# Kernel optimization log

Hardware: AMD Instinct MI355X
Metric: run time of the kernel (lower is better)

Reference implementation:

```python
import jax, jax.numpy as jnp
import numpy as np

B, S, D, H = 4, 2048, 1024, 16
DH = D // H  # 64
EPS = 1e-6


def _phi(t):
    # positive feature map used by linear attention: elu(x) + 1
    return jax.nn.elu(t) + 1.0


def setup_inputs() -> dict:
    key = jax.random.key(0)
    ks = jax.random.split(key, 5)
    scale = 1.0 / np.sqrt(D)
    return {
        "x": jax.random.normal(ks[0], (B, S, D), dtype=jnp.float32),
        "Wq": jax.random.normal(ks[1], (D, D), dtype=jnp.float32) * scale,
        "Wk": jax.random.normal(ks[2], (D, D), dtype=jnp.float32) * scale,
        "Wv": jax.random.normal(ks[3], (D, D), dtype=jnp.float32) * scale,
        "Wo": jax.random.normal(ks[4], (D, D), dtype=jnp.float32) * scale,
    }


def reference(x, Wq, Wk, Wv, Wo):
    b, s, d = x.shape
    # projections -> [b, s, H, DH]
    q = _phi((x @ Wq).reshape(b, s, H, DH))
    k = _phi((x @ Wk).reshape(b, s, H, DH))
    v = (x @ Wv).reshape(b, s, H, DH)

    # time-major for scan: [s, b, H, DH]
    qT = jnp.moveaxis(q, 1, 0)
    kT = jnp.moveaxis(k, 1, 0)
    vT = jnp.moveaxis(v, 1, 0)

    S0 = jnp.zeros((b, H, DH, DH), dtype=x.dtype)  # matrix memory per head
    z0 = jnp.zeros((b, H, DH), dtype=x.dtype)      # normalizer per head

    def step(carry, qkv):
        Smat, z = carry
        qt, kt, vt = qkv
        Smat = Smat + kt[..., :, None] * vt[..., None, :]  # [b,H,DH,DH]
        z = z + kt
        num = jnp.einsum('bhd,bhde->bhe', qt, Smat)
        den = jnp.einsum('bhd,bhd->bh', qt, z)
        out = num / (den[..., None] + EPS)
        return (Smat, z), out

    _, outs = jax.lax.scan(step, (S0, z0), (qT, kT, vT))  # [s,b,H,DH]
    out = jnp.moveaxis(outs, 0, 1).reshape(b, s, d)
    return out @ Wo
```

## Files before the change

kernel.cpp:

```cpp
#include <hip/hip_runtime.h>
#include <hip/hip_bf16.h>
#include <math.h>

constexpr int Bb  = 4;
constexpr int SEQ = 2048;
constexpr int Dd  = 1024;
constexpr int Hh  = 16;
constexpr int DHh = 64;
constexpr int Cc  = 64;
constexpr int NCc = SEQ / Cc;
constexpr int Mm  = Bb * SEQ;
constexpr float EPSf = 1e-6f;

typedef __attribute__((ext_vector_type(8))) short bf16x8;
typedef __attribute__((ext_vector_type(4))) float f32x4;
typedef __attribute__((ext_vector_type(8))) unsigned short u16x8;

__device__ __forceinline__ float bf2f(unsigned short u) {
    return __uint_as_float((unsigned)u << 16);
}
__device__ __forceinline__ unsigned short f2bf(float f) {
    unsigned u = __float_as_uint(f);
    unsigned r = u + 0x7fff + ((u >> 16) & 1);
    return (unsigned short)(r >> 16);
}
__device__ __forceinline__ int swz(int row, int col) {
    return col ^ (((row >> 3) & 7) << 3);
}

__global__ __launch_bounds__(256)
void cast_bf16(const float* __restrict__ in, unsigned short* __restrict__ out, int n8) {
    int i = blockIdx.x * 256 + threadIdx.x;
    if (i >= n8) return;
    const float4* p = reinterpret_cast<const float4*>(in) + (size_t)i * 2;
    float4 a = p[0], b = p[1];
    u16x8 o;
    o[0] = f2bf(a.x); o[1] = f2bf(a.y); o[2] = f2bf(a.z); o[3] = f2bf(a.w);
    o[4] = f2bf(b.x); o[5] = f2bf(b.y); o[6] = f2bf(b.z); o[7] = f2bf(b.w);
    *(reinterpret_cast<u16x8*>(out) + i) = o;
}

__global__ __launch_bounds__(256)
void transpose_cast_w(const float* __restrict__ W0, const float* __restrict__ W1,
                      const float* __restrict__ W2, const float* __restrict__ W3,
                      unsigned short* __restrict__ WT) {
    const float* W = (blockIdx.z == 0) ? W0 : (blockIdx.z == 1) ? W1
                     : (blockIdx.z == 2) ? W2 : W3;
    unsigned short* T = WT + (size_t)blockIdx.z * Dd * Dd;
    __shared__ float t[64][65];
    const int r0 = blockIdx.y * 64, c0 = blockIdx.x * 64;
    const int tid = threadIdx.x;
    const int lr = tid >> 4, lc4 = (tid & 15) * 4;
#pragma unroll
    for (int it = 0; it < 4; ++it) {
        int row = lr + it * 16;
        float4 v = *reinterpret_cast<const float4*>(W + (size_t)(r0 + row) * Dd + c0 + lc4);
        t[row][lc4 + 0] = v.x; t[row][lc4 + 1] = v.y;
        t[row][lc4 + 2] = v.z; t[row][lc4 + 3] = v.w;
    }
    __syncthreads();
#pragma unroll
    for (int it = 0; it < 4; ++it) {
        int col = lr + it * 16;
        ushort4 o;
        o.x = f2bf(t[lc4 + 0][col]); o.y = f2bf(t[lc4 + 1][col]);
        o.z = f2bf(t[lc4 + 2][col]); o.w = f2bf(t[lc4 + 3][col]);
        *reinterpret_cast<ushort4*>(T + (size_t)(c0 + col) * Dd + r0 + lc4) = o;
    }
}

template<int QKV>
__global__ __launch_bounds__(512, 1)
void gemm_pipe(const unsigned short* __restrict__ A, const unsigned short* __restrict__ BT,
               float* __restrict__ outF, unsigned short* __restrict__ oQ,
               unsigned short* __restrict__ oK, unsigned short* __restrict__ oV) {
    constexpr int Kd  = 1024;
    constexpr int BK  = 64;
    constexpr int NT  = Kd / BK;
    constexpr int GX  = QKV ? 12 : 4;
    constexpr int NWG = GX * 64;
    constexpr int BUFSZ = (128 + 256) * BK;

    __shared__ __align__(16) unsigned short lds[3 * BUFSZ];

    const int wg0 = blockIdx.x;
    const int wg  = (wg0 & 7) * (NWG >> 3) + (wg0 >> 3);
    const int by = wg & 63, bx = wg >> 6;
    const int row0 = by * 128;
    const int col0 = bx * 256;

    const int tid  = threadIdx.x;
    const int lane = tid & 63;
    const int wave = tid >> 6;
    const int wm = (wave >> 2) * 64;
    const int wn = (wave & 3) * 64;
    const int fr = lane & 15;
    const int hi = lane >> 4;

    f32x4 acc[4][4];
#pragma unroll
    for (int mf = 0; mf < 4; ++mf)
#pragma unroll
        for (int nf = 0; nf < 4; ++nf) acc[mf][nf] = (f32x4){0.f, 0.f, 0.f, 0.f};

    auto stage1 = [&](int sel, int kt, int l) {
        unsigned short* base = &lds[sel * BUFSZ];
        int seg = l * 512 + tid;
        if (l < 2) {
            int row = seg >> 3, sp = seg & 7;
            int gcol = kt + ((sp ^ (row & 7)) << 3);
            __builtin_amdgcn_global_load_lds(
                (const __attribute__((address_space(1))) void*)(A + (size_t)(row0 + row) * Kd + gcol),
                (__attribute__((address_space(3))) void*)(base + seg * 8), 16, 0, 0);
        } else {
            int bseg = seg - 1024;
            int row = bseg >> 3, sp = bseg & 7;
            int gcol = kt + ((sp ^ (row & 7)) << 3);
            __builtin_amdgcn_global_load_lds(
                (const __attribute__((address_space(1))) void*)(BT + (size_t)(col0 + row) * Kd + gcol),
                (__attribute__((address_space(3))) void*)(base + 8192 + bseg * 8), 16, 0, 0);
        }
    };
    auto lda = [&](const unsigned short* bufA, int mf, int ks) {
        int row = wm + mf * 16 + fr;
        int sp = ((ks << 2) | hi) ^ (row & 7);
        return *reinterpret_cast<const bf16x8*>(bufA + row * 64 + sp * 8);
    };
    auto ldb = [&](const unsigned short* bufB, int nf, int ks) {
        int row = wn + nf * 16 + fr;
        int sp = ((ks << 2) | hi) ^ (row & 7);
        return *reinterpret_cast<const bf16x8*>(bufB + row * 64 + sp * 8);
    };

#pragma unroll
    for (int l = 0; l < 6; ++l) stage1(0, 0, l);
#pragma unroll
    for (int l = 0; l < 6; ++l) stage1(1, BK, l);

    int selc = 0;
    for (int t = 0; t < NT; ++t) {
        if (t < NT - 1) { asm volatile("s_waitcnt vmcnt(6)" ::: "memory"); }
        else            { asm volatile("s_waitcnt vmcnt(0)" ::: "memory"); }
        __builtin_amdgcn_sched_barrier(0);
        __builtin_amdgcn_s_barrier();
        __builtin_amdgcn_sched_barrier(0);

        const unsigned short* bufA = &lds[selc * BUFSZ];
        const unsigned short* bufB = bufA + 8192;
        int sels = selc + 2; if (sels >= 3) sels -= 3;
        const bool st = (t + 2 < NT);
        const int kt2 = (t + 2) * BK;

        bf16x8 a0_[4], a1_[4], bL[2], bM[2], bN[2], bO[2];

#pragma unroll
        for (int mf = 0; mf < 4; ++mf) a0_[mf] = lda(bufA, mf, 0);
        bL[0] = ldb(bufB, 0, 0); bL[1] = ldb(bufB, 1, 0);
        bM[0] = ldb(bufB, 2, 0); bM[1] = ldb(bufB, 3, 0);

        asm volatile("s_waitcnt lgkmcnt(2)" ::: "memory");
        __builtin_amdgcn_sched_barrier(0);
        __builtin_amdgcn_s_setprio(1);
#pragma unroll
        for (int mf = 0; mf < 4; ++mf) {
            acc[mf][0] = __builtin_amdgcn_mfma_f32_16x16x32_bf16(a0_[mf], bL[0], acc[mf][0], 0, 0, 0);
            acc[mf][1] = __builtin_amdgcn_mfma_f32_16x16x32_bf16(a0_[mf], bL[1], acc[mf][1], 0, 0, 0);
        }
        __builtin_amdgcn_s_setprio(0);

#pragma unroll
        for (int mf = 0; mf < 4; ++mf) a1_[mf] = lda(bufA, mf, 1);
        bN[0] = ldb(bufB, 0, 1); bN[1] = ldb(bufB, 1, 1);
        if (st) { stage1(sels, kt2, 0); stage1(sels, kt2, 1); stage1(sels, kt2, 2); }

        asm volatile("s_waitcnt lgkmcnt(6)" ::: "memory");
        __builtin_amdgcn_sched_barrier(0);
        __builtin_amdgcn_s_setprio(1);
#pragma unroll
        for (int mf = 0; mf < 4; ++mf) {
            acc[mf][2] = __builtin_amdgcn_mfma_f32_16x16x32_bf16(a0_[mf], bM[0], acc[mf][2], 0, 0, 0);
            acc[mf][3] = __builtin_amdgcn_mfma_f32_16x16x32_bf16(a0_[mf], bM[1], acc[mf][3], 0, 0, 0);
        }
        __builtin_amdgcn_s_setprio(0);

        bO[0] = ldb(bufB, 2, 1); bO[1] = ldb(bufB, 3, 1);
        if (st) { stage1(sels, kt2, 3); stage1(sels, kt2, 4); stage1(sels, kt2, 5); }

        asm volatile("s_waitcnt lgkmcnt(2)" ::: "memory");
        __builtin_amdgcn_sched_barrier(0);
        __builtin_amdgcn_s_setprio(1);
#pragma unroll
        for (int mf = 0; mf < 4; ++mf) {
            acc[mf][0] = __builtin_amdgcn_mfma_f32_16x16x32_bf16(a1_[mf], bN[0], acc[mf][0], 0, 0, 0);
            acc[mf][1] = __builtin_amdgcn_mfma_f32_16x16x32_bf16(a1_[mf], bN[1], acc[mf][1], 0, 0, 0);
        }
        __builtin_amdgcn_s_setprio(0);

        asm volatile("s_waitcnt lgkmcnt(0)" ::: "memory");
        __builtin_amdgcn_sched_barrier(0);
        __builtin_amdgcn_s_setprio(1);
#pragma unroll
        for (int mf = 0; mf < 4; ++mf) {
            acc[mf][2] = __builtin_amdgcn_mfma_f32_16x16x32_bf16(a1_[mf], bO[0], acc[mf][2], 0, 0, 0);
            acc[mf][3] = __builtin_amdgcn_mfma_f32_16x16x32_bf16(a1_[mf], bO[1], acc[mf][3], 0, 0, 0);
        }
        __builtin_amdgcn_s_setprio(0);

        selc = (selc == 2) ? 0 : selc + 1;
    }

    if (QKV) {
        const int sel = col0 >> 10;
        unsigned short* ob = (sel == 0) ? oQ : (sel == 1) ? oK : oV;
        const bool phi = (sel < 2);
        const int ncol0 = col0 & 1023;
#pragma unroll
        for (int mf = 0; mf < 4; ++mf)
#pragma unroll
            for (int nf = 0; nf < 4; ++nf)
#pragma unroll
                for (int r = 0; r < 4; ++r) {
                    int orow = row0 + wm + mf * 16 + hi * 4 + r;
                    int ocol = ncol0 + wn + nf * 16 + fr;
                    float v = acc[mf][nf][r];
                    if (phi) v = (v > 0.f) ? (v + 1.f) : __expf(v);
                    ob[(size_t)orow * Dd + ocol] = f2bf(v);
                }
    } else {
#pragma unroll
        for (int mf = 0; mf < 4; ++mf)
#pragma unroll
            for (int nf = 0; nf < 4; ++nf)
#pragma unroll
                for (int r = 0; r < 4; ++r) {
                    int orow = row0 + wm + mf * 16 + hi * 4 + r;
                    int ocol = col0 + wn + nf * 16 + fr;
                    outF[(size_t)orow * Dd + ocol] = acc[mf][nf][r];
                }
    }
}

__global__ __launch_bounds__(256)
void chunk_sums_mfma(const unsigned short* __restrict__ Kb, const unsigned short* __restrict__ Vb,
                     unsigned short* __restrict__ CSb, float* __restrict__ CZ) {
    const int blk = blockIdx.x;
    const int c  = blk & (NCc - 1);
    const int bh = blk >> 5;
    const int b  = bh >> 4;
    const int h  = bh & 15;
    const int tid  = threadIdx.x;
    const int wave = tid >> 6, lane = tid & 63;
    const int lo = lane & 15, hi = lane >> 4;
    const int wr = (wave >> 1) * 32, wc = (wave & 1) * 32;

    __shared__ __align__(16) unsigned short Kt[64][72];
    __shared__ __align__(16) unsigned short Vt[64][72];

    const size_t rowbase = ((size_t)b * SEQ + c * Cc) * Dd + (size_t)h * DHh;

#pragma unroll
    for (int it = 0; it < 2; ++it) {
        int idx = tid + it * 256;
        int r = idx >> 3, c8 = (idx & 7) * 8;
        u16x8 kv = *reinterpret_cast<const u16x8*>(Kb + rowbase + (size_t)r * Dd + c8);
        u16x8 vv = *reinterpret_cast<const u16x8*>(Vb + rowbase + (size_t)r * Dd + c8);
#pragma unroll
        for (int q = 0; q < 8; ++q) {
            int d = c8 + q;
            int sc = swz(d, r);
            Kt[d][sc] = kv[q];
            Vt[d][sc] = vv[q];
        }
    }
    __syncthreads();

    f32x4 acc[2][2];
#pragma unroll
    for (int mf = 0; mf < 2; ++mf)
#pragma unroll
        for (int nf = 0; nf < 2; ++nf) acc[mf][nf] = (f32x4){0.f, 0.f, 0.f, 0.f};

#pragma unroll
    for (int kb = 0; kb < 2; ++kb) {
        const int ko = kb * 32 + hi * 8;
        bf16x8 av[2], bk[2];
#pragma unroll
        for (int mf = 0; mf < 2; ++mf) {
            int row = wr + mf * 16 + lo;
            av[mf] = *reinterpret_cast<const bf16x8*>(&Vt[row][swz(row, ko)]);
        }
#pragma unroll
        for (int nf = 0; nf < 2; ++nf) {
            int row = wc + nf * 16 + lo;
            bk[nf] = *reinterpret_cast<const bf16x8*>(&Kt[row][swz(row, ko)]);
        }
#pragma unroll
        for (int mf = 0; mf < 2; ++mf)
#pragma unroll
            for (int nf = 0; nf < 2; ++nf)
                acc[mf][nf] = __builtin_amdgcn_mfma_f32_16x16x32_bf16(av[mf], bk[nf], acc[mf][nf], 0, 0, 0);
    }

    if (tid < DHh) {
        float s = 0.f;
#pragma unroll
        for (int e8 = 0; e8 < 8; ++e8) {
            u16x8 k8 = *reinterpret_cast<const u16x8*>(&Kt[tid][e8 * 8]);
#pragma unroll
            for (int q = 0; q < 8; ++q) s += bf2f(k8[q]);
        }
        CZ[((size_t)bh * NCc + c) * DHh + tid] = s;
    }

    unsigned short* csb = CSb + ((size_t)bh * NCc + c) * (DHh * DHh);
#pragma unroll
    for (int mf = 0; mf < 2; ++mf)
#pragma unroll
        for (int nf = 0; nf < 2; ++nf)
#pragma unroll
            for (int r = 0; r < 4; ++r) {
                int e = wr + mf * 16 + hi * 4 + r;
                int d = wc + nf * 16 + lo;
                csb[e * DHh + d] = f2bf(acc[mf][nf][r]);
            }
}

__global__ __launch_bounds__(256)
void chunk_scan2(unsigned short* __restrict__ CSb, float* __restrict__ CZ) {
    const int bh = blockIdx.x >> 3;
    const int sl = blockIdx.x & 7;
    const int tid = threadIdx.x;
    const int pos = sl * 512 + tid * 2;
    float a0 = 0.f, a1 = 0.f, accz = 0.f;

    for (int c = 0; c < NCc; ++c) {
        unsigned int* p = reinterpret_cast<unsigned int*>(
            CSb + ((size_t)bh * NCc + c) * (DHh * DHh) + pos);
        unsigned int cur = *p;
        *p = (unsigned)f2bf(a0) | ((unsigned)f2bf(a1) << 16);
        a0 += bf2f((unsigned short)(cur & 0xffff));
        a1 += bf2f((unsigned short)(cur >> 16));
        if (sl == 0 && tid < DHh) {
            float* pz = CZ + ((size_t)bh * NCc + c) * DHh + tid;
            float z = *pz; *pz = accz; accz += z;
        }
    }
}

__global__ __launch_bounds__(256)
void chunk_out_mfma(const unsigned short* __restrict__ Qb, const unsigned short* __restrict__ Kb,
                    const unsigned short* __restrict__ Vb, const unsigned short* __restrict__ CSb,
                    const float* __restrict__ CZ, unsigned short* __restrict__ Ob) {
    const int blk = blockIdx.x;
    const int c  = blk & (NCc - 1);
    const int bh = blk >> 5;
    const int b  = bh >> 4;
    const int h  = bh & 15;
    const int tid  = threadIdx.x;
    const int wave = tid >> 6, lane = tid & 63;
    const int lo = lane & 15, hi = lane >> 4;
    const int wr = (wave >> 1) * 32, wc = (wave & 1) * 32;

    __shared__ __align__(16) unsigned short Qs[64][72];
    __shared__ __align__(16) unsigned short KP[64][72];
    __shared__ __align__(16) unsigned short Ss[64][72];
    __shared__ __align__(16) unsigned short Vt[64][72];
    __shared__ float zsL[DHh];
    __shared__ float rowp[64][2];
    __shared__ float denL[64];

    const size_t rowbase = ((size_t)b * SEQ + c * Cc) * Dd + (size_t)h * DHh;
    const unsigned short* csb = CSb + ((size_t)bh * NCc + c) * (DHh * DHh);

#pragma unroll
    for (int it = 0; it < 2; ++it) {
        int idx = tid + it * 256;
        int r = idx >> 3, c8 = (idx & 7) * 8;
        u16x8 qv = *reinterpret_cast<const u16x8*>(Qb + rowbase + (size_t)r * Dd + c8);
        u16x8 kv = *reinterpret_cast<const u16x8*>(Kb + rowbase + (size_t)r * Dd + c8);
        u16x8 vv = *reinterpret_cast<const u16x8*>(Vb + rowbase + (size_t)r * Dd + c8);
        u16x8 sv = *reinterpret_cast<const u16x8*>(csb + idx * 8);
        *reinterpret_cast<u16x8*>(&Qs[r][c8]) = qv;
        *reinterpret_cast<u16x8*>(&KP[r][c8]) = kv;
        *reinterpret_cast<u16x8*>(&Ss[r][c8]) = sv;
#pragma unroll
        for (int q = 0; q < 8; ++q) {
            int d = c8 + q;
            Vt[d][swz(d, r)] = vv[q];
        }
    }
    if (tid < DHh) zsL[tid] = CZ[((size_t)bh * NCc + c) * DHh + tid];
    __syncthreads();

    f32x4 accs[2][2], accO[2][2];
#pragma unroll
    for (int mf = 0; mf < 2; ++mf)
#pragma unroll
        for (int nf = 0; nf < 2; ++nf) {
            accs[mf][nf] = (f32x4){0.f, 0.f, 0.f, 0.f};
            accO[mf][nf] = (f32x4){0.f, 0.f, 0.f, 0.f};
        }

#pragma unroll
    for (int kb = 0; kb < 2; ++kb) {
        const int ko = kb * 32 + hi * 8;
        bf16x8 aq[2], bk[2], bs[2];
#pragma unroll
        for (int mf = 0; mf < 2; ++mf)
            aq[mf] = *reinterpret_cast<const bf16x8*>(&Qs[wr + mf * 16 + lo][ko]);
#pragma unroll
        for (int nf = 0; nf < 2; ++nf) {
            bk[nf] = *reinterpret_cast<const bf16x8*>(&KP[wc + nf * 16 + lo][ko]);
            bs[nf] = *reinterpret_cast<const bf16x8*>(&Ss[wc + nf * 16 + lo][ko]);
        }
#pragma unroll
        for (int mf = 0; mf < 2; ++mf)
#pragma unroll
            for (int nf = 0; nf < 2; ++nf) {
                accs[mf][nf] = __builtin_amdgcn_mfma_f32_16x16x32_bf16(aq[mf], bk[nf], accs[mf][nf], 0, 0, 0);
                accO[mf][nf] = __builtin_amdgcn_mfma_f32_16x16x32_bf16(aq[mf], bs[nf], accO[mf][nf], 0, 0, 0);
            }
    }

#pragma unroll
    for (int mf = 0; mf < 2; ++mf)
#pragma unroll
        for (int r = 0; r < 4; ++r) {
            int i = wr + mf * 16 + hi * 4 + r;
            float s = 0.f;
#pragma unroll
            for (int nf = 0; nf < 2; ++nf) {
                int j = wc + nf * 16 + lo;
                float v = (j <= i) ? accs[mf][nf][r] : 0.f;
                accs[mf][nf][r] = v;
                s += v;
            }
            s += __shfl_xor(s, 1); s += __shfl_xor(s, 2);
            s += __shfl_xor(s, 4); s += __shfl_xor(s, 8);
            if (lo == 0) rowp[i][wave & 1] = s;
        }
    __syncthreads();

#pragma unroll
    for (int mf = 0; mf < 2; ++mf)
#pragma unroll
        for (int nf = 0; nf < 2; ++nf)
#pragma unroll
            for (int r = 0; r < 4; ++r)
                KP[wr + mf * 16 + hi * 4 + r][wc + nf * 16 + lo] = f2bf(accs[mf][nf][r]);
    if (tid < 64) {
        float d = 0.f;
#pragma unroll
        for (int e8 = 0; e8 < 8; ++e8) {
            u16x8 q8 = *reinterpret_cast<const u16x8*>(&Qs[tid][e8 * 8]);
#pragma unroll
            for (int q = 0; q < 8; ++q) d += bf2f(q8[q]) * zsL[e8 * 8 + q];
        }
        denL[tid] = d + rowp[tid][0] + rowp[tid][1] + EPSf;
    }
    __syncthreads();

#pragma unroll
    for (int kb = 0; kb < 2; ++kb) {
        const int ko = kb * 32 + hi * 8;
        bf16x8 ap[2], bv[2];
#pragma unroll
        for (int mf = 0; mf < 2; ++mf)
            ap[mf] = *reinterpret_cast<const bf16x8*>(&KP[wr + mf * 16 + lo][ko]);
#pragma unroll
        for (int nf = 0; nf < 2; ++nf) {
            int row = wc + nf * 16 + lo;
            bv[nf] = *reinterpret_cast<const bf16x8*>(&Vt[row][swz(row, ko)]);
        }
#pragma unroll
        for (int mf = 0; mf < 2; ++mf)
#pragma unroll
            for (int nf = 0; nf < 2; ++nf)
                accO[mf][nf] = __builtin_amdgcn_mfma_f32_16x16x32_bf16(ap[mf], bv[nf], accO[mf][nf], 0, 0, 0);
    }

#pragma unroll
    for (int mf = 0; mf < 2; ++mf)
#pragma unroll
        for (int r = 0; r < 4; ++r) {
            int i = wr + mf * 16 + hi * 4 + r;
            float inv = 1.0f / denL[i];
#pragma unroll
            for (int nf = 0; nf < 2; ++nf) {
                int e = wc + nf * 16 + lo;
                Ob[rowbase + (size_t)i * Dd + e] = f2bf(accO[mf][nf][r] * inv);
            }
        }
}

extern "C" void kernel_launch(void* const* d_in, const int* in_sizes, int n_in,
                              void* d_out, int out_size, void* d_ws, size_t ws_size,
                              hipStream_t stream) {
    const float* x  = (const float*)d_in[0];
    const float* Wq = (const float*)d_in[1];
    const float* Wk = (const float*)d_in[2];
    const float* Wv = (const float*)d_in[3];
    const float* Wo = (const float*)d_in[4];

    const size_t NMD = (size_t)Mm * Dd;
    const size_t NW  = (size_t)Dd * Dd;
    unsigned short* xb  = (unsigned short*)d_ws;
    unsigned short* WT  = xb + NMD;
    unsigned short* Qb  = WT + 4 * NW;
    unsigned short* Kb  = Qb + NMD;
    unsigned short* Vb  = Kb + NMD;
    unsigned short* Obf = Vb + NMD;
    unsigned short* CSb = Obf + NMD;
    float* CZ = (float*)(CSb + (size_t)Bb * Hh * NCc * DHh * DHh);

    cast_bf16<<<(int)(NMD / 8 + 255) / 256, 256, 0, stream>>>(x, xb, (int)(NMD / 8));
    transpose_cast_w<<<dim3(16, 16, 4), 256, 0, stream>>>(Wq, Wk, Wv, Wo, WT);

    gemm_pipe<1><<<12 * 64, 512, 0, stream>>>(xb, WT, nullptr, Qb, Kb, Vb);

    chunk_sums_mfma<<<Bb * Hh * NCc, 256, 0, stream>>>(Kb, Vb, CSb, CZ);
    chunk_scan2<<<Bb * Hh * 8, 256, 0, stream>>>(CSb, CZ);
    chunk_out_mfma<<<Bb * Hh * NCc, 256, 0, stream>>>(Qb, Kb, Vb, CSb, CZ, Obf);

    gemm_pipe<0><<<4 * 64, 512, 0, stream>>>(Obf, WT + 3 * NW, (float*)d_out, nullptr, nullptr, nullptr);
}
```

Measured before the change: 135.9 us.

## Use 4 waves per GEMM block with 64x128 per-wave tiles

The pipelined GEMM drops from 8 waves of 64x64 tiles to 4 waves of 64x128 tiles in each 128x256 block. Each wave now holds 32 accumulator fragments and issues twice as many async global-to-LDS loads per stage, with the lgkmcnt waits resequenced around eight MFMA groups. The goal is more MFMA work per LDS fragment read, since each A fragment is reused across 8 B fragments, and less barrier and scheduling overhead. In exchange it doubles accumulator register pressure and halves the waves available to hide latency.

```diff
diff --git a/kernel.cpp b/kernel.cpp
--- a/kernel.cpp
+++ b/kernel.cpp
@@ -70,7 +70,7 @@
 }
 
 template<int QKV>
-__global__ __launch_bounds__(512, 1)
+__global__ __launch_bounds__(256, 1)
 void gemm_pipe(const unsigned short* __restrict__ A, const unsigned short* __restrict__ BT,
                float* __restrict__ outF, unsigned short* __restrict__ oQ,
                unsigned short* __restrict__ oK, unsigned short* __restrict__ oV) {
@@ -92,21 +92,21 @@
     const int tid  = threadIdx.x;
     const int lane = tid & 63;
     const int wave = tid >> 6;
-    const int wm = (wave >> 2) * 64;
-    const int wn = (wave & 3) * 64;
+    const int wm = (wave >> 1) * 64;
+    const int wn = (wave & 1) * 128;
     const int fr = lane & 15;
     const int hi = lane >> 4;
 
-    f32x4 acc[4][4];
+    f32x4 acc[4][8];
 #pragma unroll
     for (int mf = 0; mf < 4; ++mf)
 #pragma unroll
-        for (int nf = 0; nf < 4; ++nf) acc[mf][nf] = (f32x4){0.f, 0.f, 0.f, 0.f};
+        for (int nf = 0; nf < 8; ++nf) acc[mf][nf] = (f32x4){0.f, 0.f, 0.f, 0.f};
 
     auto stage1 = [&](int sel, int kt, int l) {
         unsigned short* base = &lds[sel * BUFSZ];
-        int seg = l * 512 + tid;
-        if (l < 2) {
+        int seg = l * 256 + tid;
+        if (l < 4) {
             int row = seg >> 3, sp = seg & 7;
             int gcol = kt + ((sp ^ (row & 7)) << 3);
             __builtin_amdgcn_global_load_lds(
@@ -133,13 +133,25 @@
     };
 
 #pragma unroll
-    for (int l = 0; l < 6; ++l) stage1(0, 0, l);
-#pragma unroll
-    for (int l = 0; l < 6; ++l) stage1(1, BK, l);
+    for (int l = 0; l < 12; ++l) stage1(0, 0, l);
+#pragma unroll
+    for (int l = 0; l < 12; ++l) stage1(1, BK, l);
+
+#define LGKM_SB(N)                                                        \
+    asm volatile("s_waitcnt lgkmcnt(" #N ")" ::: "memory");               \
+    __builtin_amdgcn_sched_barrier(0);
+#define MFMA8(AV, B0, B1, N0, N1)                                         \
+    __builtin_amdgcn_s_setprio(1);                                        \
+    _Pragma("unroll")                                                     \
+    for (int mf = 0; mf < 4; ++mf) {                                      \
+        acc[mf][N0] = __builtin_amdgcn_mfma_f32_16x16x32_bf16(AV[mf], B0, acc[mf][N0], 0, 0, 0); \
+        acc[mf][N1] = __builtin_amdgcn_mfma_f32_16x16x32_bf16(AV[mf], B1, acc[mf][N1], 0, 0, 0); \
+    }                                                                     \
+    __builtin_amdgcn_s_setprio(0);
 
     int selc = 0;
     for (int t = 0; t < NT; ++t) {
-        if (t < NT - 1) { asm volatile("s_waitcnt vmcnt(6)" ::: "memory"); }
+        if (t < NT - 1) { asm volatile("s_waitcnt vmcnt(12)" ::: "memory"); }
         else            { asm volatile("s_waitcnt vmcnt(0)" ::: "memory"); }
         __builtin_amdgcn_sched_barrier(0);
         __builtin_amdgcn_s_barrier();
@@ -151,63 +163,44 @@
         const bool st = (t + 2 < NT);
         const int kt2 = (t + 2) * BK;
 
-        bf16x8 a0_[4], a1_[4], bL[2], bM[2], bN[2], bO[2];
+        bf16x8 a0_[4], a1_[4], bb[8], bc[8];
 
 #pragma unroll
         for (int mf = 0; mf < 4; ++mf) a0_[mf] = lda(bufA, mf, 0);
-        bL[0] = ldb(bufB, 0, 0); bL[1] = ldb(bufB, 1, 0);
-        bM[0] = ldb(bufB, 2, 0); bM[1] = ldb(bufB, 3, 0);
-
-        asm volatile("s_waitcnt lgkmcnt(2)" ::: "memory");
-        __builtin_amdgcn_sched_barrier(0);
-        __builtin_amdgcn_s_setprio(1);
-#pragma unroll
-        for (int mf = 0; mf < 4; ++mf) {
-            acc[mf][0] = __builtin_amdgcn_mfma_f32_16x16x32_bf16(a0_[mf], bL[0], acc[mf][0], 0, 0, 0);
-            acc[mf][1] = __builtin_amdgcn_mfma_f32_16x16x32_bf16(a0_[mf], bL[1], acc[mf][1], 0, 0, 0);
-        }
-        __builtin_amdgcn_s_setprio(0);
-
+#pragma unroll
+        for (int nf = 0; nf < 8; ++nf) bb[nf] = ldb(bufB, nf, 0);
+
+        LGKM_SB(6)
+        MFMA8(a0_, bb[0], bb[1], 0, 1)
 #pragma unroll
         for (int mf = 0; mf < 4; ++mf) a1_[mf] = lda(bufA, mf, 1);
-        bN[0] = ldb(bufB, 0, 1); bN[1] = ldb(bufB, 1, 1);
-        if (st) { stage1(sels, kt2, 0); stage1(sels, kt2, 1); stage1(sels, kt2, 2); }
-
-        asm volatile("s_waitcnt lgkmcnt(6)" ::: "memory");
-        __builtin_amdgcn_sched_barrier(0);
-        __builtin_amdgcn_s_setprio(1);
-#pragma unroll
-        for (int mf = 0; mf < 4; ++mf) {
-            acc[mf][2] = __builtin_amdgcn_mfma_f32_16x16x32_bf16(a0_[mf], bM[0], acc[mf][2], 0, 0, 0);
-            acc[mf][3] = __builtin_amdgcn_mfma_f32_16x16x32_bf16(a0_[mf], bM[1], acc[mf][3], 0, 0, 0);
-        }
-        __builtin_amdgcn_s_setprio(0);
-
-        bO[0] = ldb(bufB, 2, 1); bO[1] = ldb(bufB, 3, 1);
-        if (st) { stage1(sels, kt2, 3); stage1(sels, kt2, 4); stage1(sels, kt2, 5); }
-
-        asm volatile("s_waitcnt lgkmcnt(2)" ::: "memory");
-        __builtin_amdgcn_sched_barrier(0);
-        __builtin_amdgcn_s_setprio(1);
-#pragma unroll
-        for (int mf = 0; mf < 4; ++mf) {
-            acc[mf][0] = __builtin_amdgcn_mfma_f32_16x16x32_bf16(a1_[mf], bN[0], acc[mf][0], 0, 0, 0);
-            acc[mf][1] = __builtin_amdgcn_mfma_f32_16x16x32_bf16(a1_[mf], bN[1], acc[mf][1], 0, 0, 0);
-        }
-        __builtin_amdgcn_s_setprio(0);
-
-        asm volatile("s_waitcnt lgkmcnt(0)" ::: "memory");
-        __builtin_amdgcn_sched_barrier(0);
-        __builtin_amdgcn_s_setprio(1);
-#pragma unroll
-        for (int mf = 0; mf < 4; ++mf) {
-            acc[mf][2] = __builtin_amdgcn_mfma_f32_16x16x32_bf16(a1_[mf], bO[0], acc[mf][2], 0, 0, 0);
-            acc[mf][3] = __builtin_amdgcn_mfma_f32_16x16x32_bf16(a1_[mf], bO[1], acc[mf][3], 0, 0, 0);
-        }
-        __builtin_amdgcn_s_setprio(0);
+        if (st) { stage1(sels, kt2, 0); stage1(sels, kt2, 1); stage1(sels, kt2, 2);
+                  stage1(sels, kt2, 3); stage1(sels, kt2, 4); stage1(sels, kt2, 5); }
+
+        LGKM_SB(8)
+        MFMA8(a0_, bb[2], bb[3], 2, 3)
+#pragma unroll
+        for (int nf = 0; nf < 8; ++nf) bc[nf] = ldb(bufB, nf, 1);
+        if (st) { stage1(sels, kt2, 6); stage1(sels, kt2, 7); stage1(sels, kt2, 8);
+                  stage1(sels, kt2, 9); stage1(sels, kt2, 10); stage1(sels, kt2, 11); }
+
+        LGKM_SB(14)
+        MFMA8(a0_, bb[4], bb[5], 4, 5)
+        LGKM_SB(12)
+        MFMA8(a0_, bb[6], bb[7], 6, 7)
+        LGKM_SB(6)
+        MFMA8(a1_, bc[0], bc[1], 0, 1)
+        LGKM_SB(4)
+        MFMA8(a1_, bc[2], bc[3], 2, 3)
+        LGKM_SB(2)
+        MFMA8(a1_, bc[4], bc[5], 4, 5)
+        LGKM_SB(0)
+        MFMA8(a1_, bc[6], bc[7], 6, 7)
 
         selc = (selc == 2) ? 0 : selc + 1;
     }
+#undef LGKM_SB
+#undef MFMA8
 
     if (QKV) {
         const int sel = col0 >> 10;
@@ -217,7 +210,7 @@
 #pragma unroll
         for (int mf = 0; mf < 4; ++mf)
 #pragma unroll
-            for (int nf = 0; nf < 4; ++nf)
+            for (int nf = 0; nf < 8; ++nf)
 #pragma unroll
                 for (int r = 0; r < 4; ++r) {
                     int orow = row0 + wm + mf * 16 + hi * 4 + r;
@@ -230,7 +223,7 @@
 #pragma unroll
         for (int mf = 0; mf < 4; ++mf)
 #pragma unroll
-            for (int nf = 0; nf < 4; ++nf)
+            for (int nf = 0; nf < 8; ++nf)
 #pragma unroll
                 for (int r = 0; r < 4; ++r) {
                     int orow = row0 + wm + mf * 16 + hi * 4 + r;
@@ -516,11 +509,11 @@
     cast_bf16<<<(int)(NMD / 8 + 255) / 256, 256, 0, stream>>>(x, xb, (int)(NMD / 8));
     transpose_cast_w<<<dim3(16, 16, 4), 256, 0, stream>>>(Wq, Wk, Wv, Wo, WT);
 
-    gemm_pipe<1><<<12 * 64, 512, 0, stream>>>(xb, WT, nullptr, Qb, Kb, Vb);
+    gemm_pipe<1><<<12 * 64, 256, 0, stream>>>(xb, WT, nullptr, Qb, Kb, Vb);
 
     chunk_sums_mfma<<<Bb * Hh * NCc, 256, 0, stream>>>(Kb, Vb, CSb, CZ);
     chunk_scan2<<<Bb * Hh * 8, 256, 0, stream>>>(CSb, CZ);
     chunk_out_mfma<<<Bb * Hh * NCc, 256, 0, stream>>>(Qb, Kb, Vb, CSb, CZ, Obf);
 
-    gemm_pipe<0><<<4 * 64, 512, 0, stream>>>(Obf, WT + 3 * NW, (float*)d_out, nullptr, nullptr, nullptr);
-}
+    gemm_pipe<0><<<4 * 64, 256, 0, stream>>>(Obf, WT + 3 * NW, (float*)d_out, nullptr, nullptr, nullptr);
+}
```

Result: slower. 169.6 us (+24.8%).

## Switch projection GEMMs to 256x256 tiles with double-buffered LDS pipeline

Applied to the files above, without the earlier changes.

Replaces the 128x256-tile triple-buffered GEMM with a 256x256-tile kernel where each wave computes a 128x64 sub-tile. The A and B LDS loads are interleaved in halves across the MFMA phases, using two buffers instead of three. Larger tiles double the reuse of each loaded B fragment and cut global traffic per flop. In exchange the grid shrinks (384 and 128 workgroups on 256 CUs), which leaves the output projection under-filling the GPU and raises register pressure despite launch_bounds(512,2).

```diff
diff --git a/kernel.cpp b/kernel.cpp
--- a/kernel.cpp
+++ b/kernel.cpp
@@ -70,59 +70,55 @@
 }
 
 template<int QKV>
-__global__ __launch_bounds__(512, 1)
-void gemm_pipe(const unsigned short* __restrict__ A, const unsigned short* __restrict__ BT,
-               float* __restrict__ outF, unsigned short* __restrict__ oQ,
-               unsigned short* __restrict__ oK, unsigned short* __restrict__ oV) {
+__global__ __launch_bounds__(512, 2)
+void gemm_256(const unsigned short* __restrict__ A, const unsigned short* __restrict__ BT,
+              float* __restrict__ outF, unsigned short* __restrict__ oQ,
+              unsigned short* __restrict__ oK, unsigned short* __restrict__ oV) {
     constexpr int Kd  = 1024;
     constexpr int BK  = 64;
     constexpr int NT  = Kd / BK;
     constexpr int GX  = QKV ? 12 : 4;
-    constexpr int NWG = GX * 64;
-    constexpr int BUFSZ = (128 + 256) * BK;
-
-    __shared__ __align__(16) unsigned short lds[3 * BUFSZ];
+    constexpr int NWG = GX * 32;
+    constexpr int BUFSZ = 512 * 64;
+
+    __shared__ __align__(16) unsigned short lds[2 * BUFSZ];
 
     const int wg0 = blockIdx.x;
     const int wg  = (wg0 & 7) * (NWG >> 3) + (wg0 >> 3);
-    const int by = wg & 63, bx = wg >> 6;
-    const int row0 = by * 128;
+    const int by = wg & 31, bx = wg >> 5;
+    const int row0 = by * 256;
     const int col0 = bx * 256;
 
     const int tid  = threadIdx.x;
     const int lane = tid & 63;
     const int wave = tid >> 6;
-    const int wm = (wave >> 2) * 64;
+    const int wm = (wave >> 2) * 128;
     const int wn = (wave & 3) * 64;
     const int fr = lane & 15;
     const int hi = lane >> 4;
 
-    f32x4 acc[4][4];
-#pragma unroll
-    for (int mf = 0; mf < 4; ++mf)
+    f32x4 acc[8][4];
+#pragma unroll
+    for (int mf = 0; mf < 8; ++mf)
 #pragma unroll
         for (int nf = 0; nf < 4; ++nf) acc[mf][nf] = (f32x4){0.f, 0.f, 0.f, 0.f};
 
-    auto stage1 = [&](int sel, int kt, int l) {
-        unsigned short* base = &lds[sel * BUFSZ];
-        int seg = l * 512 + tid;
-        if (l < 2) {
-            int row = seg >> 3, sp = seg & 7;
-            int gcol = kt + ((sp ^ (row & 7)) << 3);
-            __builtin_amdgcn_global_load_lds(
-                (const __attribute__((address_space(1))) void*)(A + (size_t)(row0 + row) * Kd + gcol),
-                (__attribute__((address_space(3))) void*)(base + seg * 8), 16, 0, 0);
-        } else {
-            int bseg = seg - 1024;
-            int row = bseg >> 3, sp = bseg & 7;
-            int gcol = kt + ((sp ^ (row & 7)) << 3);
-            __builtin_amdgcn_global_load_lds(
-                (const __attribute__((address_space(1))) void*)(BT + (size_t)(col0 + row) * Kd + gcol),
-                (__attribute__((address_space(3))) void*)(base + 8192 + bseg * 8), 16, 0, 0);
-        }
+    auto stageA = [&](int sel, int kt, int p) {
+        int row = p * 64 + (tid >> 3), sp = tid & 7;
+        int gcol = kt + ((sp ^ (row & 7)) << 3);
+        __builtin_amdgcn_global_load_lds(
+            (const __attribute__((address_space(1))) void*)(A + (size_t)(row0 + row) * Kd + gcol),
+            (__attribute__((address_space(3))) void*)(lds + sel * BUFSZ + p * 4096 + tid * 8), 16, 0, 0);
     };
-    auto lda = [&](const unsigned short* bufA, int mf, int ks) {
-        int row = wm + mf * 16 + fr;
+    auto stageB = [&](int sel, int kt, int p) {
+        int row = p * 64 + (tid >> 3), sp = tid & 7;
+        int gcol = kt + ((sp ^ (row & 7)) << 3);
+        __builtin_amdgcn_global_load_lds(
+            (const __attribute__((address_space(1))) void*)(BT + (size_t)(col0 + row) * Kd + gcol),
+            (__attribute__((address_space(3))) void*)(lds + sel * BUFSZ + 16384 + p * 4096 + tid * 8), 16, 0, 0);
+    };
+    auto lda = [&](const unsigned short* bufA, int mfA, int ks) {
+        int row = wm + mfA * 16 + fr;
         int sp = ((ks << 2) | hi) ^ (row & 7);
         return *reinterpret_cast<const bf16x8*>(bufA + row * 64 + sp * 8);
     };
@@ -132,82 +128,114 @@
         return *reinterpret_cast<const bf16x8*>(bufB + row * 64 + sp * 8);
     };
 
-#pragma unroll
-    for (int l = 0; l < 6; ++l) stage1(0, 0, l);
-#pragma unroll
-    for (int l = 0; l < 6; ++l) stage1(1, BK, l);
-
-    int selc = 0;
+#define SB0 __builtin_amdgcn_sched_barrier(0);
+#define VMW(N) asm volatile("s_waitcnt vmcnt(" #N ")" ::: "memory");
+#define LGW(N) asm volatile("s_waitcnt lgkmcnt(" #N ")" ::: "memory");
+
+    stageA(0, 0, 0); stageA(0, 0, 2); SB0
+    stageB(0, 0, 0); stageB(0, 0, 2); SB0
+    stageB(0, 0, 1); stageB(0, 0, 3); SB0
+    stageA(0, 0, 1); stageA(0, 0, 3);
+
+    bf16x8 aH[4][2], b01[2][2], b23[2][2];
+
     for (int t = 0; t < NT; ++t) {
-        if (t < NT - 1) { asm volatile("s_waitcnt vmcnt(6)" ::: "memory"); }
-        else            { asm volatile("s_waitcnt vmcnt(0)" ::: "memory"); }
-        __builtin_amdgcn_sched_barrier(0);
-        __builtin_amdgcn_s_barrier();
-        __builtin_amdgcn_sched_barrier(0);
-
-        const unsigned short* bufA = &lds[selc * BUFSZ];
-        const unsigned short* bufB = bufA + 8192;
-        int sels = selc + 2; if (sels >= 3) sels -= 3;
-        const bool st = (t + 2 < NT);
-        const int kt2 = (t + 2) * BK;
-
-        bf16x8 a0_[4], a1_[4], bL[2], bM[2], bN[2], bO[2];
-
-#pragma unroll
-        for (int mf = 0; mf < 4; ++mf) a0_[mf] = lda(bufA, mf, 0);
-        bL[0] = ldb(bufB, 0, 0); bL[1] = ldb(bufB, 1, 0);
-        bM[0] = ldb(bufB, 2, 0); bM[1] = ldb(bufB, 3, 0);
-
-        asm volatile("s_waitcnt lgkmcnt(2)" ::: "memory");
-        __builtin_amdgcn_sched_barrier(0);
-        __builtin_amdgcn_s_setprio(1);
-#pragma unroll
-        for (int mf = 0; mf < 4; ++mf) {
-            acc[mf][0] = __builtin_amdgcn_mfma_f32_16x16x32_bf16(a0_[mf], bL[0], acc[mf][0], 0, 0, 0);
-            acc[mf][1] = __builtin_amdgcn_mfma_f32_16x16x32_bf16(a0_[mf], bL[1], acc[mf][1], 0, 0, 0);
-        }
-        __builtin_amdgcn_s_setprio(0);
-
-#pragma unroll
-        for (int mf = 0; mf < 4; ++mf) a1_[mf] = lda(bufA, mf, 1);
-        bN[0] = ldb(bufB, 0, 1); bN[1] = ldb(bufB, 1, 1);
-        if (st) { stage1(sels, kt2, 0); stage1(sels, kt2, 1); stage1(sels, kt2, 2); }
-
-        asm volatile("s_waitcnt lgkmcnt(6)" ::: "memory");
-        __builtin_amdgcn_sched_barrier(0);
-        __builtin_amdgcn_s_setprio(1);
-#pragma unroll
-        for (int mf = 0; mf < 4; ++mf) {
-            acc[mf][2] = __builtin_amdgcn_mfma_f32_16x16x32_bf16(a0_[mf], bM[0], acc[mf][2], 0, 0, 0);
-            acc[mf][3] = __builtin_amdgcn_mfma_f32_16x16x32_bf16(a0_[mf], bM[1], acc[mf][3], 0, 0, 0);
-        }
-        __builtin_amdgcn_s_setprio(0);
-
-        bO[0] = ldb(bufB, 2, 1); bO[1] = ldb(bufB, 3, 1);
-        if (st) { stage1(sels, kt2, 3); stage1(sels, kt2, 4); stage1(sels, kt2, 5); }
-
-        asm volatile("s_waitcnt lgkmcnt(2)" ::: "memory");
-        __builtin_amdgcn_sched_barrier(0);
-        __builtin_amdgcn_s_setprio(1);
-#pragma unroll
-        for (int mf = 0; mf < 4; ++mf) {
-            acc[mf][0] = __builtin_amdgcn_mfma_f32_16x16x32_bf16(a1_[mf], bN[0], acc[mf][0], 0, 0, 0);
-            acc[mf][1] = __builtin_amdgcn_mfma_f32_16x16x32_bf16(a1_[mf], bN[1], acc[mf][1], 0, 0, 0);
-        }
-        __builtin_amdgcn_s_setprio(0);
-
-        asm volatile("s_waitcnt lgkmcnt(0)" ::: "memory");
-        __builtin_amdgcn_sched_barrier(0);
-        __builtin_amdgcn_s_setprio(1);
-#pragma unroll
-        for (int mf = 0; mf < 4; ++mf) {
-            acc[mf][2] = __builtin_amdgcn_mfma_f32_16x16x32_bf16(a1_[mf], bO[0], acc[mf][2], 0, 0, 0);
-            acc[mf][3] = __builtin_amdgcn_mfma_f32_16x16x32_bf16(a1_[mf], bO[1], acc[mf][3], 0, 0, 0);
-        }
-        __builtin_amdgcn_s_setprio(0);
-
-        selc = (selc == 2) ? 0 : selc + 1;
-    }
+        const int selc = t & 1, ss = selc ^ 1;
+        const unsigned short* bufA = lds + selc * BUFSZ;
+        const unsigned short* bufB = bufA + 16384;
+        const int kt1 = (t + 1) * BK;
+        const bool st = (t + 1 < NT);
+
+        VMW(6) SB0
+        __builtin_amdgcn_s_barrier(); SB0
+#pragma unroll
+        for (int m = 0; m < 4; ++m) aH[m][0] = lda(bufA, m, 0);
+#pragma unroll
+        for (int m = 0; m < 4; ++m) aH[m][1] = lda(bufA, m, 1);
+        VMW(2) SB0
+        __builtin_amdgcn_s_barrier(); SB0
+        b01[0][0] = ldb(bufB, 0, 0); b01[1][0] = ldb(bufB, 1, 0);
+        b01[0][1] = ldb(bufB, 0, 1); b01[1][1] = ldb(bufB, 1, 1);
+        if (st) { stageA(ss, kt1, 0); stageA(ss, kt1, 2); }
+        LGW(2) SB0
+        __builtin_amdgcn_s_setprio(1);
+#pragma unroll
+        for (int m = 0; m < 4; ++m) {
+            acc[m][0] = __builtin_amdgcn_mfma_f32_16x16x32_bf16(aH[m][0], b01[0][0], acc[m][0], 0, 0, 0);
+            acc[m][1] = __builtin_amdgcn_mfma_f32_16x16x32_bf16(aH[m][0], b01[1][0], acc[m][1], 0, 0, 0);
+        }
+        __builtin_amdgcn_s_setprio(0);
+        LGW(0) SB0
+        __builtin_amdgcn_s_setprio(1);
+#pragma unroll
+        for (int m = 0; m < 4; ++m) {
+            acc[m][0] = __builtin_amdgcn_mfma_f32_16x16x32_bf16(aH[m][1], b01[0][1], acc[m][0], 0, 0, 0);
+            acc[m][1] = __builtin_amdgcn_mfma_f32_16x16x32_bf16(aH[m][1], b01[1][1], acc[m][1], 0, 0, 0);
+        }
+        __builtin_amdgcn_s_setprio(0);
+
+        b23[0][0] = ldb(bufB, 2, 0); b23[1][0] = ldb(bufB, 3, 0);
+        b23[0][1] = ldb(bufB, 2, 1); b23[1][1] = ldb(bufB, 3, 1);
+        if (st) { stageB(ss, kt1, 0); stageB(ss, kt1, 2); }
+        LGW(2) SB0
+        __builtin_amdgcn_s_setprio(1);
+#pragma unroll
+        for (int m = 0; m < 4; ++m) {
+            acc[m][2] = __builtin_amdgcn_mfma_f32_16x16x32_bf16(aH[m][0], b23[0][0], acc[m][2], 0, 0, 0);
+            acc[m][3] = __builtin_amdgcn_mfma_f32_16x16x32_bf16(aH[m][0], b23[1][0], acc[m][3], 0, 0, 0);
+        }
+        __builtin_amdgcn_s_setprio(0);
+        LGW(0) SB0
+        __builtin_amdgcn_s_setprio(1);
+#pragma unroll
+        for (int m = 0; m < 4; ++m) {
+            acc[m][2] = __builtin_amdgcn_mfma_f32_16x16x32_bf16(aH[m][1], b23[0][1], acc[m][2], 0, 0, 0);
+            acc[m][3] = __builtin_amdgcn_mfma_f32_16x16x32_bf16(aH[m][1], b23[1][1], acc[m][3], 0, 0, 0);
+        }
+        __builtin_amdgcn_s_setprio(0);
+
+        if (st) { VMW(4) } else { VMW(0) }
+        SB0
+        __builtin_amdgcn_s_barrier(); SB0
+#pragma unroll
+        for (int m = 0; m < 4; ++m) aH[m][0] = lda(bufA, m + 4, 0);
+#pragma unroll
+        for (int m = 0; m < 4; ++m) aH[m][1] = lda(bufA, m + 4, 1);
+        if (st) { stageB(ss, kt1, 1); stageB(ss, kt1, 3); }
+        LGW(4) SB0
+        __builtin_amdgcn_s_setprio(1);
+#pragma unroll
+        for (int m = 0; m < 4; ++m) {
+            acc[m + 4][0] = __builtin_amdgcn_mfma_f32_16x16x32_bf16(aH[m][0], b01[0][0], acc[m + 4][0], 0, 0, 0);
+            acc[m + 4][1] = __builtin_amdgcn_mfma_f32_16x16x32_bf16(aH[m][0], b01[1][0], acc[m + 4][1], 0, 0, 0);
+        }
+        __builtin_amdgcn_s_setprio(0);
+        LGW(0) SB0
+        __builtin_amdgcn_s_setprio(1);
+#pragma unroll
+        for (int m = 0; m < 4; ++m) {
+            acc[m + 4][0] = __builtin_amdgcn_mfma_f32_16x16x32_bf16(aH[m][1], b01[0][1], acc[m + 4][0], 0, 0, 0);
+            acc[m + 4][1] = __builtin_amdgcn_mfma_f32_16x16x32_bf16(aH[m][1], b01[1][1], acc[m + 4][1], 0, 0, 0);
+        }
+        __builtin_amdgcn_s_setprio(0);
+
+        if (st) { stageA(ss, kt1, 1); stageA(ss, kt1, 3); }
+        __builtin_amdgcn_s_setprio(1);
+#pragma unroll
+        for (int m = 0; m < 4; ++m) {
+            acc[m + 4][2] = __builtin_amdgcn_mfma_f32_16x16x32_bf16(aH[m][0], b23[0][0], acc[m + 4][2], 0, 0, 0);
+            acc[m + 4][3] = __builtin_amdgcn_mfma_f32_16x16x32_bf16(aH[m][0], b23[1][0], acc[m + 4][3], 0, 0, 0);
+        }
+#pragma unroll
+        for (int m = 0; m < 4; ++m) {
+            acc[m + 4][2] = __builtin_amdgcn_mfma_f32_16x16x32_bf16(aH[m][1], b23[0][1], acc[m + 4][2], 0, 0, 0);
+            acc[m + 4][3] = __builtin_amdgcn_mfma_f32_16x16x32_bf16(aH[m][1], b23[1][1], acc[m + 4][3], 0, 0, 0);
+        }
+        __builtin_amdgcn_s_setprio(0);
+    }
+#undef SB0
+#undef VMW
+#undef LGW
 
     if (QKV) {
         const int sel = col0 >> 10;
@@ -215,7 +243,7 @@
         const bool phi = (sel < 2);
         const int ncol0 = col0 & 1023;
 #pragma unroll
-        for (int mf = 0; mf < 4; ++mf)
+        for (int mf = 0; mf < 8; ++mf)
 #pragma unroll
             for (int nf = 0; nf < 4; ++nf)
 #pragma unroll
@@ -228,7 +256,7 @@
                 }
     } else {
 #pragma unroll
-        for (int mf = 0; mf < 4; ++mf)
+        for (int mf = 0; mf < 8; ++mf)
 #pragma unroll
             for (int nf = 0; nf < 4; ++nf)
 #pragma unroll
@@ -516,11 +544,11 @@
     cast_bf16<<<(int)(NMD / 8 + 255) / 256, 256, 0, stream>>>(x, xb, (int)(NMD / 8));
     transpose_cast_w<<<dim3(16, 16, 4), 256, 0, stream>>>(Wq, Wk, Wv, Wo, WT);
 
-    gemm_pipe<1><<<12 * 64, 512, 0, stream>>>(xb, WT, nullptr, Qb, Kb, Vb);
+    gemm_256<1><<<12 * 32, 512, 0, stream>>>(xb, WT, nullptr, Qb, Kb, Vb);
 
     chunk_sums_mfma<<<Bb * Hh * NCc, 256, 0, stream>>>(Kb, Vb, CSb, CZ);
     chunk_scan2<<<Bb * Hh * 8, 256, 0, stream>>>(CSb, CZ);
     chunk_out_mfma<<<Bb * Hh * NCc, 256, 0, stream>>>(Qb, Kb, Vb, CSb, CZ, Obf);
 
-    gemm_pipe<0><<<4 * 64, 512, 0, stream>>>(Obf, WT + 3 * NW, (float*)d_out, nullptr, nullptr, nullptr);
-}
+    gemm_256<0><<<4 * 32, 512, 0, stream>>>(Obf, WT + 3 * NW, (float*)d_out, nullptr, nullptr, nullptr);
+}
```

New measurement: 149.8 us. +10.2%, slower.
